# Kernel tuning notes

Hardware: AMD Instinct MI355X
Metric: run time of the kernel (lower is better)

## Reference

```python
import jax, jax.numpy as jnp
import numpy as np
from jax.ops import segment_sum

N_NODES = 100000
N_EDGES = 3200000
NUM_FEATURES = 256


def setup_inputs() -> dict:
    key = jax.random.key(0)
    ks = jax.random.split(key, 12)
    def lin(k, fan_in, fan_out):
        bound = 1.0 / np.sqrt(fan_in)
        kw, kb = jax.random.split(k)
        W = jax.random.uniform(kw, (fan_in, fan_out), jnp.float32, -bound, bound)
        b = jax.random.uniform(kb, (fan_out,), jnp.float32, -bound, bound)
        return W, b
    x = jax.random.normal(ks[0], (N_NODES, NUM_FEATURES), jnp.float32)
    edge_index = jax.random.randint(ks[1], (2, N_EDGES), 0, N_NODES, jnp.int64 if jax.config.jax_enable_x64 else jnp.int32)
    W1, b1 = lin(ks[2], NUM_FEATURES, 64)
    W2, b2 = lin(ks[3], 64, 32)
    W3, b3 = lin(ks[4], 32, 16)
    Ws02, bs02 = lin(ks[5], NUM_FEATURES, 32)
    Ws03, bs03 = lin(ks[6], NUM_FEATURES, 16)
    Ws13, bs13 = lin(ks[7], 64, 16)
    Wout, bout = lin(ks[8], 16, 1)
    return dict(x=x, edge_index=edge_index, W1=W1, b1=b1, W2=W2, b2=b2,
                W3=W3, b3=b3, Ws02=Ws02, bs02=bs02, Ws03=Ws03, bs03=bs03,
                Ws13=Ws13, bs13=bs13, Wout=Wout, bout=bout)


def _deg_inv_sqrt(edge_index, n_nodes):
    # gcn_norm with self-loops: degree counted at target nodes, +1 for self-loop
    dst = edge_index[1]
    deg = segment_sum(jnp.ones(edge_index.shape[1], jnp.float32), dst, num_segments=n_nodes) + 1.0
    return jnp.where(deg > 0, jax.lax.rsqrt(deg), 0.0)


def _gcn_conv(x, W, b, edge_index, dinv):
    # PyG GCNConv: h = x W; out[i] = sum_{j->i} dinv[j]*dinv[i]*h[j] + dinv[i]^2*h[i] + b
    src, dst = edge_index[0], edge_index[1]
    h = x @ W                                   # [N, out]
    norm = (dinv[src] * dinv[dst])[:, None]     # [E, 1]
    agg = segment_sum(h[src] * norm, dst, num_segments=x.shape[0])
    agg = agg + (dinv * dinv)[:, None] * h      # self-loop term
    return agg + b


def reference(x, edge_index, W1, b1, W2, b2, W3, b3,
              Ws02, bs02, Ws03, bs03, Ws13, bs13, Wout, bout):
    # Dropout in eval mode (identity).
    dinv = _deg_inv_sqrt(edge_index, x.shape[0])
    x1 = jax.nn.relu(_gcn_conv(x, W1, b1, edge_index, dinv))
    x2 = jax.nn.relu(_gcn_conv(x1, W2, b2, edge_index, dinv) + x @ Ws02 + bs02)
    x3 = jax.nn.relu(_gcn_conv(x2, W3, b3, edge_index, dinv)
                     + x @ Ws03 + bs03 + x1 @ Ws13 + bs13)
    return jax.nn.sigmoid(x3 @ Wout + bout)
```

## Files before the change

kernel.cpp:

```cpp
#include <hip/hip_runtime.h>
#include <hip/hip_bf16.h>
#include <math.h>


#define NBUCK_MAX 512
#define P1_CHUNK 8192
#define EPT 32
#define BCAP 9216
#define PREP_BLOCKS 142
#define HIST_BLOCKS 1024

typedef __attribute__((ext_vector_type(8))) short bfrag;
typedef __attribute__((ext_vector_type(4))) float f4_t;
typedef __attribute__((ext_vector_type(2))) float f2_t;

__device__ inline float uaf(unsigned u) { return __uint_as_float(u); }
__device__ inline ushort f2bf(float f) {
    __hip_bfloat16 b = __float2bfloat16(f);
    return *reinterpret_cast<ushort*>(&b);
}
__device__ inline bfrag cvt8(const float4 a, const float4 b) {
    union { ushort u[8]; bfrag f; } r;
    r.u[0] = f2bf(a.x); r.u[1] = f2bf(a.y); r.u[2] = f2bf(a.z); r.u[3] = f2bf(a.w);
    r.u[4] = f2bf(b.x); r.u[5] = f2bf(b.y); r.u[6] = f2bf(b.z); r.u[7] = f2bf(b.w);
    return r.f;
}
__device__ inline bfrag ld_bfrag(const ushort* p) {
    const uint4 raw = *reinterpret_cast<const uint4*>(p);
    return *reinterpret_cast<const bfrag*>(&raw);
}


__global__ __launch_bounds__(256) void fka_kernel(
    const float* __restrict__ W1, const float* __restrict__ Ws02,
    const float* __restrict__ Ws03, const float* __restrict__ W2,
    const float* __restrict__ Ws13, const float* __restrict__ W3,
    ushort* __restrict__ Wt0, ushort* __restrict__ Wt1, ushort* __restrict__ Wt2,
    const int* __restrict__ dst, int E, int* __restrict__ bucket_count,
    int nbuckets)
{
    if (blockIdx.x < PREP_BLOCKS) {
        const int idx = blockIdx.x * 256 + threadIdx.x;
        if (idx < 32768) {
            int f = idx >> 8, k = idx & 255;
            float v = 0.f;
            if (f < 64)       v = W1[k * 64 + f];
            else if (f < 96)  v = Ws02[k * 32 + (f - 64)];
            else if (f < 112) v = Ws03[k * 16 + (f - 96)];
            Wt0[idx] = f2bf(v);
        } else if (idx < 32768 + 3072) {
            int t = idx - 32768;
            int f = t >> 6, k = t & 63;
            float v = (f < 32) ? W2[k * 32 + f] : Ws13[k * 16 + (f - 32)];
            Wt1[t] = f2bf(v);
        } else if (idx < 32768 + 3072 + 512) {
            int t = idx - 32768 - 3072;
            int f = t >> 5, k = t & 31;
            Wt2[t] = f2bf(W3[k * 16 + f]);
        }
        return;
    }
    __shared__ int lhist[NBUCK_MAX];
    const int bid = blockIdx.x - PREP_BLOCKS;
    for (int i = threadIdx.x; i < nbuckets; i += 256) lhist[i] = 0;
    __syncthreads();
    const int stride = HIST_BLOCKS * 256;
    for (int e = bid * 256 + threadIdx.x; e < E; e += stride)
        atomicAdd(&lhist[dst[e] >> 8], 1);
    __syncthreads();
    for (int i = threadIdx.x; i < nbuckets; i += 256) {
        int c = lhist[i];
        if (c) atomicAdd(&bucket_count[i], c);
    }
}


__global__ __launch_bounds__(512) void bucket_scan_kernel(
    const int* __restrict__ bucket_count, int* __restrict__ bucket_base,
    int* __restrict__ bucket_cursor, int nbuckets)
{
    __shared__ int tmp[512];
    const int tid = threadIdx.x;
    int v = (tid < nbuckets) ? bucket_count[tid] : 0;
    tmp[tid] = v;
    __syncthreads();
    for (int off = 1; off < 512; off <<= 1) {
        int t = (tid >= off) ? tmp[tid - off] : 0;
        __syncthreads();
        tmp[tid] += t;
        __syncthreads();
    }
    if (tid < nbuckets) {
        int base = tmp[tid] - v;
        bucket_base[tid]   = base;
        bucket_cursor[tid] = base;
    }
}


__global__ __launch_bounds__(256) void partition_kernel(
    const int* __restrict__ src, const int* __restrict__ dst, int E,
    int* __restrict__ bucket_cursor, unsigned int* __restrict__ keys, int nbuckets)
{
    __shared__ int hist[NBUCK_MAX];
    __shared__ int lofs[NBUCK_MAX];
    __shared__ int gbase[NBUCK_MAX];
    __shared__ int lcur[NBUCK_MAX];
    __shared__ int ssum[256];
    __shared__ unsigned int stage[P1_CHUNK];
    __shared__ int gidx[P1_CHUNK];

    const int tid = threadIdx.x;
    const int e0  = blockIdx.x * P1_CHUNK;
    const int nE  = min(P1_CHUNK, E - e0);

    for (int i = tid; i < NBUCK_MAX; i += 256) { hist[i] = 0; lcur[i] = 0; }
    __syncthreads();

    int myb[EPT];
    unsigned int mypk[EPT];
#pragma unroll
    for (int j = 0; j < EPT; ++j) {
        const int e = e0 + tid + j * 256;
        if (e < E) {
            const int d = dst[e];
            myb[j]  = d >> 8;
            mypk[j] = ((unsigned int)(d & 255) << 17) | (unsigned int)src[e];
            atomicAdd(&hist[myb[j]], 1);
        } else myb[j] = -1;
    }
    __syncthreads();

    int a0 = (2 * tid     < nbuckets) ? hist[2 * tid]     : 0;
    int a1 = (2 * tid + 1 < nbuckets) ? hist[2 * tid + 1] : 0;
    ssum[tid] = a0 + a1;
    __syncthreads();
    for (int off = 1; off < 256; off <<= 1) {
        int t = (tid >= off) ? ssum[tid - off] : 0;
        __syncthreads();
        ssum[tid] += t;
        __syncthreads();
    }
    const int ex = ssum[tid] - (a0 + a1);
    if (2 * tid     < nbuckets) lofs[2 * tid]     = ex;
    if (2 * tid + 1 < nbuckets) lofs[2 * tid + 1] = ex + a0;
    __syncthreads();

    for (int i = tid; i < nbuckets; i += 256)
        gbase[i] = atomicAdd(&bucket_cursor[i], hist[i]);
    __syncthreads();

#pragma unroll
    for (int j = 0; j < EPT; ++j) {
        if (myb[j] >= 0) {
            const int b = myb[j];
            const int l = lofs[b] + atomicAdd(&lcur[b], 1);
            stage[l] = mypk[j];
            gidx[l]  = gbase[b] - lofs[b] + l;
        }
    }
    __syncthreads();

    for (int i = tid; i < nE; i += 256)
        keys[gidx[i]] = stage[i];
}


__global__ __launch_bounds__(256) void csr_build_kernel(
    const unsigned int* __restrict__ keys, const int* __restrict__ bucket_base,
    const int* __restrict__ bucket_count,
    int* __restrict__ row_off, float* __restrict__ dinv, int* __restrict__ col,
    int N, int E)
{
    __shared__ unsigned int inb[BCAP];
    __shared__ int outv[BCAP];
    __shared__ int hist[256];
    __shared__ int lofs[256];
    __shared__ int ssum[256];

    const int tid  = threadIdx.x;
    const int b    = blockIdx.x;
    const int base = bucket_base[b];
    const int cnt  = min(bucket_count[b], BCAP);
    const int n0   = b << 8;
    const int nn   = min(256, N - n0);

    for (int i = tid; i < cnt; i += 256) inb[i] = keys[base + i];
    hist[tid] = 0;
    __syncthreads();

    for (int i = tid; i < cnt; i += 256)
        atomicAdd(&hist[inb[i] >> 17], 1);
    __syncthreads();

    ssum[tid] = hist[tid];
    __syncthreads();
    for (int off = 1; off < 256; off <<= 1) {
        int t = (tid >= off) ? ssum[tid - off] : 0;
        __syncthreads();
        ssum[tid] += t;
        __syncthreads();
    }
    lofs[tid] = ssum[tid] - hist[tid];

    if (tid < nn) {
        row_off[n0 + tid] = base + lofs[tid];
        dinv[n0 + tid]    = rsqrtf((float)hist[tid] + 1.0f);
    }
    if (b == 0 && tid == 0) row_off[N] = E;
    __syncthreads();

    hist[tid] = 0;
    __syncthreads();

    for (int i = tid; i < cnt; i += 256) {
        const unsigned int k = inb[i];
        const int node = k >> 17;
        const int l = lofs[node] + atomicAdd(&hist[node], 1);
        outv[l] = (int)(k & 0x1FFFF);
    }
    __syncthreads();

    for (int i = tid; i < cnt; i += 256)
        col[base + i] = outv[i];
}


__global__ __launch_bounds__(256, 3) void gemm_mfma0(
    const float* __restrict__ X, const ushort* __restrict__ Wt0,
    const float* __restrict__ bs02, const float* __restrict__ bs03,
    const float* __restrict__ dinv,
    ushort* __restrict__ g1, float* __restrict__ pre2,
    float* __restrict__ pre3, int N)
{
    __shared__ __align__(16) float Xs[2][64 * 64];

    const int tid  = threadIdx.x;
    const int lane = tid & 63;
    const int wf   = tid >> 6;
    const int n0   = blockIdx.x * 64;
    const int mrow = lane & 15;
    const int q    = lane >> 4;
    const int kq   = q * 8;

    bfrag bfr[2][8];
#pragma unroll
    for (int ft = 0; ft < 2; ++ft) {
        const ushort* wr = &Wt0[(size_t)(wf * 32 + ft * 16 + mrow) * 256 + kq];
#pragma unroll
        for (int p = 0; p < 8; ++p)
            bfr[ft][p] = ld_bfrag(&wr[p * 32]);
    }

    int srow[4], schunk[4];
#pragma unroll
    for (int j = 0; j < 4; ++j) {
        const int R = wf * 16 + j * 4 + q;
        srow[j]   = min(n0 + R, N - 1);
        schunk[j] = mrow ^ (R & 7);
    }

    auto STAGE = [&](int buf, int kc) {
#pragma unroll
        for (int j = 0; j < 4; ++j) {
            const float* gsrc =
                X + (size_t)srow[j] * 256 + kc * 64 + schunk[j] * 4;
            __builtin_amdgcn_global_load_lds(
                (const __attribute__((address_space(1))) unsigned int*)gsrc,
                (__attribute__((address_space(3))) unsigned int*)
                    &Xs[buf][(wf * 16 + j * 4) * 64],
                16, 0, 0);
        }
    };

    f4_t acc[4][2];
#pragma unroll
    for (int a = 0; a < 4; ++a)
#pragma unroll
        for (int b = 0; b < 2; ++b) acc[a][b] = {0.f, 0.f, 0.f, 0.f};

    STAGE(0, 0);
    __syncthreads();

    int cur = 0;
    for (int kc = 0; kc < 4; ++kc) {
        if (kc < 3) STAGE(cur ^ 1, kc + 1);
        const float4* Xs4 = reinterpret_cast<const float4*>(&Xs[cur][0]);
#pragma unroll
        for (int pl = 0; pl < 2; ++pl) {
            bfrag af[4];
#pragma unroll
            for (int mt = 0; mt < 4; ++mt) {
                const int r  = mt * 16 + mrow;
                const int c0 = pl * 8 + q * 2;
                const float4 u0 = Xs4[r * 16 + (c0 ^ (r & 7))];
                const float4 u1 = Xs4[r * 16 + ((c0 + 1) ^ (r & 7))];
                af[mt] = cvt8(u0, u1);
            }
            const int pg = kc * 2 + pl;
#pragma unroll
            for (int mt = 0; mt < 4; ++mt)
#pragma unroll
                for (int ft = 0; ft < 2; ++ft)
                    acc[mt][ft] = __builtin_amdgcn_mfma_f32_16x16x32_bf16(
                        af[mt], bfr[ft][pg], acc[mt][ft], 0, 0, 0);
        }
        __syncthreads();
        cur ^= 1;
    }

    char* sm = (char*)Xs;
    ushort* g1s = (ushort*)sm;
    float*  p2s = (float*)(sm + 8192);
    float*  p3s = (float*)(sm + 16384);

    if (wf < 2) {
#pragma unroll
        for (int mt = 0; mt < 4; ++mt) {
#pragma unroll
            for (int r = 0; r < 4; ++r) {
                const int nl = mt * 16 + q * 4 + r;
                const float di = dinv[min(n0 + nl, N - 1)];
#pragma unroll
                for (int ft = 0; ft < 2; ++ft)
                    g1s[nl * 64 + wf * 32 + ft * 16 + mrow] =
                        f2bf(di * acc[mt][ft][r]);
            }
        }
    } else if (wf == 2) {
#pragma unroll
        for (int mt = 0; mt < 4; ++mt)
#pragma unroll
            for (int ft = 0; ft < 2; ++ft)
#pragma unroll
                for (int r = 0; r < 4; ++r)
                    p2s[(mt * 16 + q * 4 + r) * 32 + ft * 16 + mrow] =
                        acc[mt][ft][r] + bs02[ft * 16 + mrow];
    } else {
#pragma unroll
        for (int mt = 0; mt < 4; ++mt)
#pragma unroll
            for (int r = 0; r < 4; ++r)
                p3s[(mt * 16 + q * 4 + r) * 16 + mrow] =
                    acc[mt][0][r] + bs03[mrow];
    }
    __syncthreads();

    const uint4* g1v = (const uint4*)g1s;
    const uint4* p2v = (const uint4*)p2s;
    const uint4* p3v = (const uint4*)p3s;
#pragma unroll
    for (int t = 0; t < 2; ++t) {
        const int i   = t * 256 + tid;
        const int row = i >> 3;
        if (n0 + row < N)
            *(uint4*)(g1 + (size_t)(n0 + row) * 64 + (i & 7) * 8) = g1v[i];
    }
#pragma unroll
    for (int t = 0; t < 2; ++t) {
        const int i   = t * 256 + tid;
        const int row = i >> 3;
        if (n0 + row < N)
            *(uint4*)(pre2 + (size_t)(n0 + row) * 32 + (i & 7) * 4) = p2v[i];
    }
    {
        const int i   = tid;
        const int row = i >> 2;
        if (n0 + row < N)
            *(uint4*)(pre3 + (size_t)(n0 + row) * 16 + (i & 3) * 4) = p3v[i];
    }
}


__global__ __launch_bounds__(256) void gemm_mfma1(
    const ushort* __restrict__ X1, const ushort* __restrict__ Wt1,
    const float* __restrict__ bs13, const float* __restrict__ dinv,
    __hip_bfloat16* __restrict__ g2, float* __restrict__ pre3, int N)
{
    __shared__ __align__(16) ushort g2s[128 * 32];
    __shared__ __align__(16) float  p3s[128 * 16];

    const int tid  = threadIdx.x;
    const int lane = tid & 63;
    const int wave = tid >> 6;
    const int nb   = blockIdx.x * 128;
    const int n0   = nb + wave * 32;
    const int mrow = lane & 15;
    const int q    = lane >> 4;
    const int kq   = q * 8;

    f4_t acc[2][3];
#pragma unroll
    for (int a = 0; a < 2; ++a)
#pragma unroll
        for (int b = 0; b < 3; ++b) acc[a][b] = {0.f, 0.f, 0.f, 0.f};

    const ushort* xrow[2];
#pragma unroll
    for (int mt = 0; mt < 2; ++mt) {
        int r = n0 + mt * 16 + mrow;
        r = (r < N) ? r : (N - 1);
        xrow[mt] = &X1[(size_t)r * 64 + kq];
    }
    const ushort* wrow[3];
#pragma unroll
    for (int ft = 0; ft < 3; ++ft)
        wrow[ft] = &Wt1[(size_t)(ft * 16 + mrow) * 64 + kq];

#pragma unroll
    for (int p = 0; p < 2; ++p) {
        bfrag af[2], bf[3];
#pragma unroll
        for (int mt = 0; mt < 2; ++mt) af[mt] = ld_bfrag(&xrow[mt][p * 32]);
#pragma unroll
        for (int ft = 0; ft < 3; ++ft) bf[ft] = ld_bfrag(&wrow[ft][p * 32]);
#pragma unroll
        for (int mt = 0; mt < 2; ++mt)
#pragma unroll
            for (int ft = 0; ft < 3; ++ft)
                acc[mt][ft] = __builtin_amdgcn_mfma_f32_16x16x32_bf16(
                    af[mt], bf[ft], acc[mt][ft], 0, 0, 0);
    }

#pragma unroll
    for (int mt = 0; mt < 2; ++mt) {
#pragma unroll
        for (int r = 0; r < 4; ++r) {
            const int nl = wave * 32 + mt * 16 + q * 4 + r;
            const float di = dinv[min(nb + nl, N - 1)];
            g2s[nl * 32 +      mrow] = f2bf(di * acc[mt][0][r]);
            g2s[nl * 32 + 16 + mrow] = f2bf(di * acc[mt][1][r]);
            p3s[nl * 16 + mrow] = acc[mt][2][r] + bs13[mrow];
        }
    }
    __syncthreads();

    const uint4*  g2v = (const uint4*)g2s;
    const float4* p3v = (const float4*)p3s;
#pragma unroll
    for (int t = 0; t < 2; ++t) {
        const int i   = t * 256 + tid;
        const int row = i >> 2;
        if (nb + row < N)
            *(uint4*)((ushort*)g2 + (size_t)(nb + row) * 32 + (i & 3) * 8) =
                g2v[i];
    }
#pragma unroll
    for (int t = 0; t < 2; ++t) {
        const int i   = t * 256 + tid;
        const int row = i >> 2;
        if (nb + row < N) {
            float4* dst =
                (float4*)(pre3 + (size_t)(nb + row) * 16 + (i & 3) * 4);
            float4 v = *dst;
            const float4 s = p3v[i];
            v.x += s.x; v.y += s.y; v.z += s.z; v.w += s.w;
            *dst = v;
        }
    }
}


template<int F, int MODE>
__global__ __launch_bounds__(256) void agg_kernel(
    const ushort* __restrict__ g, const float* __restrict__ dinv,
    const int* __restrict__ row_off, const int* __restrict__ col,
    const float* __restrict__ bias, const float* __restrict__ pre,
    const ushort* __restrict__ Wk,
    const float* __restrict__ Wout, const float* __restrict__ bout,
    void* __restrict__ out, int N)
{
    constexpr int FG  = F / 8;
    constexpr int EPW = 64 / FG;
    constexpr int U   = 32 / EPW;
    constexpr int LSH = (F == 64) ? 7 : (F == 32 ? 6 : 5);

    const int lane = threadIdx.x & 63;
    const int wv   = threadIdx.x >> 6;
    const int i    = blockIdx.x * 4 + wv;
    if (i >= N) return;

    const int fg  = lane & (FG - 1);
    const int eo  = lane / FG;
    const unsigned fbb = (unsigned)fg * 16;

    const char* gb = (const char*)g;

    f2_t acc0 = {0.f, 0.f}, acc1 = {0.f, 0.f};
    f2_t acc2 = {0.f, 0.f}, acc3 = {0.f, 0.f};

    const int s = row_off[i], e = row_off[i + 1];
    const int nfull = (e - s) >> 5;
    int p = s;
    const int* cp = col + s + eo;

    for (int it = 0; it < nfull; ++it, p += 32, cp += 32) {
        unsigned voff[U];
#pragma unroll
        for (int u = 0; u < U; ++u)
            voff[u] = ((unsigned)cp[u * EPW] << LSH) + fbb;
        uint4 w[U];
#pragma unroll
        for (int u = 0; u < U; ++u)
            w[u] = *reinterpret_cast<const uint4*>(gb + voff[u]);
#pragma unroll
        for (int u = 0; u < U; ++u) {
            acc0 += (f2_t){uaf(w[u].x << 16), uaf(w[u].x & 0xffff0000u)};
            acc1 += (f2_t){uaf(w[u].y << 16), uaf(w[u].y & 0xffff0000u)};
            acc2 += (f2_t){uaf(w[u].z << 16), uaf(w[u].z & 0xffff0000u)};
            acc3 += (f2_t){uaf(w[u].w << 16), uaf(w[u].w & 0xffff0000u)};
        }
    }
    if (p < e) {
        float m[U];
        unsigned voff[U];
#pragma unroll
        for (int u = 0; u < U; ++u) {
            const int q = p + eo + u * EPW;
            m[u]    = (q < e) ? 1.0f : 0.0f;
            voff[u] = ((unsigned)col[min(q, e - 1)] << LSH) + fbb;
        }
        uint4 w[U];
#pragma unroll
        for (int u = 0; u < U; ++u)
            w[u] = *reinterpret_cast<const uint4*>(gb + voff[u]);
#pragma unroll
        for (int u = 0; u < U; ++u) {
            const f2_t mm = {m[u], m[u]};
            acc0 += mm * (f2_t){uaf(w[u].x << 16), uaf(w[u].x & 0xffff0000u)};
            acc1 += mm * (f2_t){uaf(w[u].y << 16), uaf(w[u].y & 0xffff0000u)};
            acc2 += mm * (f2_t){uaf(w[u].z << 16), uaf(w[u].z & 0xffff0000u)};
            acc3 += mm * (f2_t){uaf(w[u].w << 16), uaf(w[u].w & 0xffff0000u)};
        }
    }

#pragma unroll
    for (int ro = FG; ro < 64; ro <<= 1) {
        acc0.x += __shfl_xor(acc0.x, ro); acc0.y += __shfl_xor(acc0.y, ro);
        acc1.x += __shfl_xor(acc1.x, ro); acc1.y += __shfl_xor(acc1.y, ro);
        acc2.x += __shfl_xor(acc2.x, ro); acc2.y += __shfl_xor(acc2.y, ro);
        acc3.x += __shfl_xor(acc3.x, ro); acc3.y += __shfl_xor(acc3.y, ro);
    }

    const uint4 ws =
        *reinterpret_cast<const uint4*>(gb + (((unsigned)i) << LSH) + fbb);
    const float di = dinv[i];
    const int fb = fg * 8;
    const float4 b0 = *reinterpret_cast<const float4*>(&bias[fb]);
    const float4 b1 = *reinterpret_cast<const float4*>(&bias[fb + 4]);

    float v0 = di * (acc0.x + uaf(ws.x << 16))         + b0.x;
    float v1 = di * (acc0.y + uaf(ws.x & 0xffff0000u)) + b0.y;
    float v2 = di * (acc1.x + uaf(ws.y << 16))         + b0.z;
    float v3 = di * (acc1.y + uaf(ws.y & 0xffff0000u)) + b0.w;
    float v4 = di * (acc2.x + uaf(ws.z << 16))         + b1.x;
    float v5 = di * (acc2.y + uaf(ws.z & 0xffff0000u)) + b1.y;
    float v6 = di * (acc3.x + uaf(ws.w << 16))         + b1.z;
    float v7 = di * (acc3.y + uaf(ws.w & 0xffff0000u)) + b1.w;

    if (MODE != 0) {
        const float4 p0 = *reinterpret_cast<const float4*>(&pre[(size_t)i * F + fb]);
        const float4 p1 = *reinterpret_cast<const float4*>(&pre[(size_t)i * F + fb + 4]);
        v0 += p0.x; v1 += p0.y; v2 += p0.z; v3 += p0.w;
        v4 += p1.x; v5 += p1.y; v6 += p1.z; v7 += p1.w;
    }
    v0 = fmaxf(v0, 0.f); v1 = fmaxf(v1, 0.f);
    v2 = fmaxf(v2, 0.f); v3 = fmaxf(v3, 0.f);
    v4 = fmaxf(v4, 0.f); v5 = fmaxf(v5, 0.f);
    v6 = fmaxf(v6, 0.f); v7 = fmaxf(v7, 0.f);

    if (MODE == 0) {
        if (lane < FG) {
            uint4 o;
            o.x = (unsigned)f2bf(v0) | ((unsigned)f2bf(v1) << 16);
            o.y = (unsigned)f2bf(v2) | ((unsigned)f2bf(v3) << 16);
            o.z = (unsigned)f2bf(v4) | ((unsigned)f2bf(v5) << 16);
            o.w = (unsigned)f2bf(v6) | ((unsigned)f2bf(v7) << 16);
            *reinterpret_cast<uint4*>((char*)out + (((size_t)i) << LSH) + fbb) = o;
        }
    } else if (MODE == 1) {
        const uint4 wr = *reinterpret_cast<const uint4*>(&Wk[eo * 32 + fb]);
        float sacc;
        sacc  = v0 * uaf(wr.x << 16);
        sacc += v1 * uaf(wr.x & 0xffff0000u);
        sacc += v2 * uaf(wr.y << 16);
        sacc += v3 * uaf(wr.y & 0xffff0000u);
        sacc += v4 * uaf(wr.z << 16);
        sacc += v5 * uaf(wr.z & 0xffff0000u);
        sacc += v6 * uaf(wr.w << 16);
        sacc += v7 * uaf(wr.w & 0xffff0000u);
        sacc += __shfl_xor(sacc, 1);
        sacc += __shfl_xor(sacc, 2);
        if ((lane & 3) == 0)
            ((ushort*)out)[(size_t)i * 16 + eo] = f2bf(di * sacc);
    } else {
        const float4 w0 = *reinterpret_cast<const float4*>(&Wout[fb]);
        const float4 w1 = *reinterpret_cast<const float4*>(&Wout[fb + 4]);
        float t = v0 * w0.x + v1 * w0.y + v2 * w0.z + v3 * w0.w +
                  v4 * w1.x + v5 * w1.y + v6 * w1.z + v7 * w1.w;
        t += __shfl_xor(t, 1);
        if (lane == 0)
            ((float*)out)[i] = 1.0f / (1.0f + expf(-(t + bout[0])));
    }
}


extern "C" void kernel_launch(void* const* d_in, const int* in_sizes, int n_in,
                              void* d_out, int out_size, void* d_ws, size_t ws_size,
                              hipStream_t stream)
{
    const float* x    = (const float*)d_in[0];
    const int*   edge = (const int*)d_in[1];
    const float* W1   = (const float*)d_in[2];
    const float* b1   = (const float*)d_in[3];
    const float* W2   = (const float*)d_in[4];
    const float* b2   = (const float*)d_in[5];
    const float* W3   = (const float*)d_in[6];
    const float* b3   = (const float*)d_in[7];
    const float* Ws02 = (const float*)d_in[8];
    const float* bs02 = (const float*)d_in[9];
    const float* Ws03 = (const float*)d_in[10];
    const float* bs03 = (const float*)d_in[11];
    const float* Ws13 = (const float*)d_in[12];
    const float* bs13 = (const float*)d_in[13];
    const float* Wout = (const float*)d_in[14];
    const float* bout = (const float*)d_in[15];

    const int N = in_sizes[0] / 256;
    const int E = in_sizes[1] / 2;
    const int* srcv = edge;
    const int* dstv = edge + E;
    const int nbuckets = (N + 255) >> 8;

    char* ws = (char*)d_ws;
    size_t off = 0;
    auto alloc = [&](size_t bytes) -> void* {
        void* p = ws + off;
        off += (bytes + 255) & ~(size_t)255;
        return p;
    };
    unsigned int* keys = (unsigned int*)alloc((size_t)E * 4);
    int*   col      = (int*)  alloc((size_t)E * 4);
    int*   bcount   = (int*)  alloc((size_t)NBUCK_MAX * 4);
    int*   bbase    = (int*)  alloc((size_t)NBUCK_MAX * 4);
    int*   bcursor  = (int*)  alloc((size_t)NBUCK_MAX * 4);
    int*   row_off  = (int*)  alloc((size_t)(N + 1) * 4);
    float* dinv     = (float*)alloc((size_t)N * 4);
    ushort* Wt0     = (ushort*)alloc((size_t)128 * 256 * 2);
    ushort* Wt1     = (ushort*)alloc((size_t)48 * 64 * 2);
    ushort* Wt2     = (ushort*)alloc((size_t)16 * 32 * 2);
    ushort* g1      = (ushort*)alloc((size_t)N * 64 * 2);
    ushort* x1      = (ushort*)alloc((size_t)N * 64 * 2);
    ushort* g2      = (ushort*)alloc((size_t)N * 32 * 2);
    ushort* g3      = (ushort*)alloc((size_t)N * 16 * 2);
    float* pre2     = (float*)alloc((size_t)N * 32 * 4);
    float* pre3     = (float*)alloc((size_t)N * 16 * 4);

    hipMemsetAsync(bcount, 0, (size_t)NBUCK_MAX * 4, stream);

    fka_kernel<<<PREP_BLOCKS + HIST_BLOCKS, 256, 0, stream>>>(
        W1, Ws02, Ws03, W2, Ws13, W3, Wt0, Wt1, Wt2,
        dstv, E, bcount, nbuckets);

    bucket_scan_kernel<<<1, 512, 0, stream>>>(bcount, bbase, bcursor, nbuckets);

    partition_kernel<<<(E + P1_CHUNK - 1) / P1_CHUNK, 256, 0, stream>>>(
        srcv, dstv, E, bcursor, keys, nbuckets);

    csr_build_kernel<<<nbuckets, 256, 0, stream>>>(
        keys, bbase, bcount, row_off, dinv, col, N, E);

    gemm_mfma0<<<(N + 63) / 64, 256, 0, stream>>>(
        x, Wt0, bs02, bs03, dinv, g1, pre2, pre3, N);

    const int ab = (N + 3) / 4;

    agg_kernel<64, 0><<<ab, 256, 0, stream>>>(
        g1, dinv, row_off, col, b1, nullptr, nullptr,
        nullptr, nullptr, x1, N);
    gemm_mfma1<<<(N + 127) / 128, 256, 0, stream>>>(
        x1, Wt1, bs13, dinv, (__hip_bfloat16*)g2, pre3, N);
    agg_kernel<32, 1><<<ab, 256, 0, stream>>>(
        g2, dinv, row_off, col, b2, pre2, Wt2,
        nullptr, nullptr, g3, N);
    agg_kernel<16, 2><<<ab, 256, 0, stream>>>(
        g3, dinv, row_off, col, b3, pre3, nullptr,
        Wout, bout, d_out, N);
}
```

Before: 419.7 us.

## Fold bucket scan into partition kernel and drop LDS staging in CSR build

The separate single-block bucket scan launch is removed. The first partition block to take a ticket now computes the bucket prefix sum and publishes it through a release flag, and every block spin-waits on that flag before claiming global offsets. The CSR build kernel no longer stages keys and sorted columns in shared memory. It reads keys from global memory twice and scatters columns straight to global memory, which frees LDS (and possibly raises occupancy) and removes the BCAP cap, in exchange for uncoalesced writes and an extra pass over global memory. The spin-wait relies on the ticket-holding block making progress, which holds in practice because it takes the ticket before spinning.

Result: slower. 435.7 us (+3.8%).

```diff
diff --git a/kernel.cpp b/kernel.cpp
--- a/kernel.cpp
+++ b/kernel.cpp
@@ -6,7 +6,6 @@
 #define NBUCK_MAX 512
 #define P1_CHUNK 8192
 #define EPT 32
-#define BCAP 9216
 #define PREP_BLOCKS 142
 #define HIST_BLOCKS 1024
 
@@ -75,32 +74,12 @@
 }
 
 
-__global__ __launch_bounds__(512) void bucket_scan_kernel(
-    const int* __restrict__ bucket_count, int* __restrict__ bucket_base,
-    int* __restrict__ bucket_cursor, int nbuckets)
-{
-    __shared__ int tmp[512];
-    const int tid = threadIdx.x;
-    int v = (tid < nbuckets) ? bucket_count[tid] : 0;
-    tmp[tid] = v;
-    __syncthreads();
-    for (int off = 1; off < 512; off <<= 1) {
-        int t = (tid >= off) ? tmp[tid - off] : 0;
-        __syncthreads();
-        tmp[tid] += t;
-        __syncthreads();
-    }
-    if (tid < nbuckets) {
-        int base = tmp[tid] - v;
-        bucket_base[tid]   = base;
-        bucket_cursor[tid] = base;
-    }
-}
-
-
 __global__ __launch_bounds__(256) void partition_kernel(
     const int* __restrict__ src, const int* __restrict__ dst, int E,
-    int* __restrict__ bucket_cursor, unsigned int* __restrict__ keys, int nbuckets)
+    const int* __restrict__ bucket_count, int* __restrict__ bucket_base,
+    int* __restrict__ bucket_cursor, int* __restrict__ ticket,
+    int* __restrict__ scan_flag,
+    unsigned int* __restrict__ keys, int nbuckets)
 {
     __shared__ int hist[NBUCK_MAX];
     __shared__ int lofs[NBUCK_MAX];
@@ -109,13 +88,41 @@
     __shared__ int ssum[256];
     __shared__ unsigned int stage[P1_CHUNK];
     __shared__ int gidx[P1_CHUNK];
+    __shared__ int am_first;
 
     const int tid = threadIdx.x;
     const int e0  = blockIdx.x * P1_CHUNK;
     const int nE  = min(P1_CHUNK, E - e0);
 
     for (int i = tid; i < NBUCK_MAX; i += 256) { hist[i] = 0; lcur[i] = 0; }
-    __syncthreads();
+    if (tid == 0) am_first = (atomicAdd(ticket, 1) == 0);
+    __syncthreads();
+
+    if (am_first) {
+        int c0 = (2 * tid     < nbuckets) ? bucket_count[2 * tid]     : 0;
+        int c1 = (2 * tid + 1 < nbuckets) ? bucket_count[2 * tid + 1] : 0;
+        ssum[tid] = c0 + c1;
+        __syncthreads();
+        for (int off = 1; off < 256; off <<= 1) {
+            int t = (tid >= off) ? ssum[tid - off] : 0;
+            __syncthreads();
+            ssum[tid] += t;
+            __syncthreads();
+        }
+        const int ex = ssum[tid] - (c0 + c1);
+        if (2 * tid < nbuckets) {
+            bucket_base[2 * tid]   = ex;
+            bucket_cursor[2 * tid] = ex;
+        }
+        if (2 * tid + 1 < nbuckets) {
+            bucket_base[2 * tid + 1]   = ex + c0;
+            bucket_cursor[2 * tid + 1] = ex + c0;
+        }
+        __syncthreads();
+        if (tid == 0)
+            __hip_atomic_store(scan_flag, 1, __ATOMIC_RELEASE,
+                               __HIP_MEMORY_SCOPE_AGENT);
+    }
 
     int myb[EPT];
     unsigned int mypk[EPT];
@@ -146,6 +153,12 @@
     if (2 * tid + 1 < nbuckets) lofs[2 * tid + 1] = ex + a0;
     __syncthreads();
 
+    if (tid == 0) {
+        while (__hip_atomic_load(scan_flag, __ATOMIC_ACQUIRE,
+                                 __HIP_MEMORY_SCOPE_AGENT) == 0) {}
+    }
+    __syncthreads();
+
     for (int i = tid; i < nbuckets; i += 256)
         gbase[i] = atomicAdd(&bucket_cursor[i], hist[i]);
     __syncthreads();
@@ -172,8 +185,6 @@
     int* __restrict__ row_off, float* __restrict__ dinv, int* __restrict__ col,
     int N, int E)
 {
-    __shared__ unsigned int inb[BCAP];
-    __shared__ int outv[BCAP];
     __shared__ int hist[256];
     __shared__ int lofs[256];
     __shared__ int ssum[256];
@@ -181,16 +192,15 @@
     const int tid  = threadIdx.x;
     const int b    = blockIdx.x;
     const int base = bucket_base[b];
-    const int cnt  = min(bucket_count[b], BCAP);
+    const int cnt  = bucket_count[b];
     const int n0   = b << 8;
     const int nn   = min(256, N - n0);
 
-    for (int i = tid; i < cnt; i += 256) inb[i] = keys[base + i];
     hist[tid] = 0;
     __syncthreads();
 
     for (int i = tid; i < cnt; i += 256)
-        atomicAdd(&hist[inb[i] >> 17], 1);
+        atomicAdd(&hist[keys[base + i] >> 17], 1);
     __syncthreads();
 
     ssum[tid] = hist[tid];
@@ -214,15 +224,11 @@
     __syncthreads();
 
     for (int i = tid; i < cnt; i += 256) {
-        const unsigned int k = inb[i];
+        const unsigned int k = keys[base + i];
         const int node = k >> 17;
         const int l = lofs[node] + atomicAdd(&hist[node], 1);
-        outv[l] = (int)(k & 0x1FFFF);
-    }
-    __syncthreads();
-
-    for (int i = tid; i < cnt; i += 256)
-        col[base + i] = outv[i];
+        col[base + l] = (int)(k & 0x1FFFF);
+    }
 }
 
 
@@ -642,6 +648,7 @@
     unsigned int* keys = (unsigned int*)alloc((size_t)E * 4);
     int*   col      = (int*)  alloc((size_t)E * 4);
     int*   bcount   = (int*)  alloc((size_t)NBUCK_MAX * 4);
+    int*   flags    = (int*)  alloc(256);
     int*   bbase    = (int*)  alloc((size_t)NBUCK_MAX * 4);
     int*   bcursor  = (int*)  alloc((size_t)NBUCK_MAX * 4);
     int*   row_off  = (int*)  alloc((size_t)(N + 1) * 4);
@@ -656,16 +663,15 @@
     float* pre2     = (float*)alloc((size_t)N * 32 * 4);
     float* pre3     = (float*)alloc((size_t)N * 16 * 4);
 
-    hipMemsetAsync(bcount, 0, (size_t)NBUCK_MAX * 4, stream);
+    hipMemsetAsync(bcount, 0, (size_t)NBUCK_MAX * 4 + 256, stream);
 
     fka_kernel<<<PREP_BLOCKS + HIST_BLOCKS, 256, 0, stream>>>(
         W1, Ws02, Ws03, W2, Ws13, W3, Wt0, Wt1, Wt2,
         dstv, E, bcount, nbuckets);
 
-    bucket_scan_kernel<<<1, 512, 0, stream>>>(bcount, bbase, bcursor, nbuckets);
-
     partition_kernel<<<(E + P1_CHUNK - 1) / P1_CHUNK, 256, 0, stream>>>(
-        srcv, dstv, E, bcursor, keys, nbuckets);
+        srcv, dstv, E, bcount, bbase, bcursor,
+        &flags[0], &flags[1], keys, nbuckets);
 
     csr_build_kernel<<<nbuckets, 256, 0, stream>>>(
         keys, bbase, bcount, row_off, dinv, col, N, E);
```
